# Kernel optimization log

Hardware: AMD Instinct MI355X
Metric: run time of the kernel (lower is better)

The kernel has to match this reference:

```python
import jax, jax.numpy as jnp
import numpy as np

N = 50000
E = 640000
IN_DIM = 23
HID = 128
NUM_CLASS = 12


def setup_inputs() -> dict:
    key = jax.random.key(0)
    ks = jax.random.split(key, 12)
    x = jax.random.normal(ks[0], (N, IN_DIM), dtype=jnp.float32)
    edge_index = jax.random.randint(ks[1], (2, E), 0, N, dtype=jnp.int32)

    def glorot(k, shape):
        fan_in, fan_out = shape
        lim = np.sqrt(6.0 / (fan_in + fan_out)).astype(np.float32)
        return jax.random.uniform(k, shape, jnp.float32, -lim, lim)

    W1 = glorot(ks[2], (IN_DIM, HID)); b1 = jnp.zeros((HID,), jnp.float32)
    W2 = glorot(ks[3], (HID, HID));    b2 = jnp.zeros((HID,), jnp.float32)
    W3 = glorot(ks[4], (HID, HID));    b3 = jnp.zeros((HID,), jnp.float32)
    Wc1 = glorot(ks[5], (HID, 64));    bc1 = jnp.zeros((64,), jnp.float32)
    Wc2 = glorot(ks[6], (64, NUM_CLASS)); bc2 = jnp.zeros((NUM_CLASS,), jnp.float32)
    return {"x": x, "edge_index": edge_index,
            "W1": W1, "b1": b1, "W2": W2, "b2": b2, "W3": W3, "b3": b3,
            "Wc1": Wc1, "bc1": bc1, "Wc2": Wc2, "bc2": bc2}


def _gcn_norm(edge_index, n_nodes):
    # add self loops, compute symmetric normalization D^-1/2 (A+I) D^-1/2
    loop = jnp.arange(n_nodes, dtype=edge_index.dtype)
    src = jnp.concatenate([edge_index[0], loop])
    dst = jnp.concatenate([edge_index[1], loop])
    deg = jax.ops.segment_sum(jnp.ones_like(dst, dtype=jnp.float32), dst,
                              num_segments=n_nodes)
    dinv = jax.lax.rsqrt(deg)  # deg >= 1 due to self loops
    norm = dinv[src] * dinv[dst]  # [E + N]
    return src, dst, norm


def _gcn_layer(h, W, b, src, dst, norm, n_nodes):
    h = h @ W                          # linear (bias applied after aggregation, per PyG)
    msg = h[src] * norm[:, None]       # gather + scale
    out = jax.ops.segment_sum(msg, dst, num_segments=n_nodes)  # scatter-add
    return out + b


def reference(x, edge_index, W1, b1, W2, b2, W3, b3, Wc1, bc1, Wc2, bc2):
    n = x.shape[0]
    src, dst, norm = _gcn_norm(edge_index, n)
    h = jnp.tanh(_gcn_layer(x, W1, b1, src, dst, norm, n))
    h = jnp.tanh(_gcn_layer(h, W2, b2, src, dst, norm, n))
    h = jnp.tanh(_gcn_layer(h, W3, b3, src, dst, norm, n))
    # dropout is identity in eval mode
    out = h @ Wc1 + bc1
    out = out @ Wc2 + bc2
    return out
```

## Files before the change

### kernel.cpp

```cpp
#include <hip/hip_runtime.h>
#include <math.h>

#define NN 50000
#define EE 640000
#define IND 23
#define HID 128
#define MIDD 64
#define NCLS 12
#define NB 49
#define QS 32766.0f
#define INVQS (1.0f / 32766.0f)
#define BSH 7
#define NBK 391
#define CHUNK 4096
#define NPB 157
#define PADB 6250

typedef short short8v __attribute__((ext_vector_type(8)));
typedef float f32x4 __attribute__((ext_vector_type(4)));
typedef unsigned long long u64;

__device__ __forceinline__ short f2bf(float f) {
    unsigned u = __float_as_uint(f);
    unsigned r = (u + 0x7FFFu + ((u >> 16) & 1u)) >> 16;
    return (short)r;
}
__device__ __forceinline__ float bf2f(short s) {
    return __uint_as_float(((unsigned)(unsigned short)s) << 16);
}

__global__ __launch_bounds__(256) void k_pre(const int* __restrict__ dst,
                                             int* __restrict__ cnt,
                                             const float* __restrict__ Wc1,
                                             const float* __restrict__ bc1,
                                             const float* __restrict__ Wc2,
                                             const float* __restrict__ bc2,
                                             float* __restrict__ Wcc,
                                             float* __restrict__ bcc,
                                             const float* __restrict__ W2,
                                             const float* __restrict__ W3,
                                             short* __restrict__ w2hi,
                                             short* __restrict__ w2lo,
                                             short* __restrict__ w3hi,
                                             short* __restrict__ w3lo) {
    const int bid = blockIdx.x;
    const int tid = threadIdx.x;
    if (bid < 2500) {
        int i = bid * 256 + tid;
        if (i < EE) atomicAdd(&cnt[dst[i]], 1);
        return;
    }
    if (bid < 2506) {
        int t = (bid - 2500) * 256 + tid;
        if (t < HID * NCLS) {
            int k = t / NCLS, c = t % NCLS;
            float s = 0.f;
#pragma unroll 8
            for (int j = 0; j < MIDD; ++j) s += Wc1[k * MIDD + j] * Wc2[j * NCLS + c];
            Wcc[t] = s;
        }
        if (t < NCLS) {
            float s = bc2[t];
#pragma unroll 8
            for (int j = 0; j < MIDD; ++j) s += bc1[j] * Wc2[j * NCLS + t];
            bcc[t] = s;
        }
        return;
    }
    int bb = bid - 2506;
    const float* W = (bb < 64) ? W2 : W3;
    short* hi = (bb < 64) ? w2hi : w3hi;
    short* lo = (bb < 64) ? w2lo : w3lo;
    int i = (bb & 63) * 256 + tid;
    int k = i >> 7, c = i & 127;
    float w = W[i];
    short h = f2bf(w);
    short l = f2bf(w - bf2f(h));
    hi[((k >> 3) * 128 + c) * 8 + (k & 7)] = h;
    lo[((k >> 3) * 128 + c) * 8 + (k & 7)] = l;
}

__global__ __launch_bounds__(256) void k_scan_local(const int* __restrict__ cnt,
                                                    int* __restrict__ row_ptr,
                                                    float* __restrict__ dinv,
                                                    int* __restrict__ sums) {
    __shared__ int wtot[4];
    const int tid = threadIdx.x;
    const int wid = tid >> 6, lane = tid & 63;
    const int base = blockIdx.x * 1024 + tid * 4;
    int v[4];
#pragma unroll
    for (int t = 0; t < 4; ++t) {
        int i = base + t;
        v[t] = (i < NN) ? cnt[i] : 0;
        if (i < NN) dinv[i] = rsqrtf((float)v[t] + 1.0f);
    }
    int slocal = v[0] + v[1] + v[2] + v[3];
    int val = slocal;
#pragma unroll
    for (int off = 1; off < 64; off <<= 1) {
        int t = __shfl_up(val, off, 64);
        if (lane >= off) val += t;
    }
    if (lane == 63) wtot[wid] = val;
    __syncthreads();
    int woff = 0;
#pragma unroll
    for (int w = 0; w < 4; ++w) woff += (w < wid) ? wtot[w] : 0;
    int run = woff + val - slocal;
#pragma unroll
    for (int t = 0; t < 4; ++t) {
        int i = base + t;
        if (i < NN) row_ptr[i] = run;
        run += v[t];
    }
    if (tid == 255) sums[blockIdx.x] = woff + val;
}

__global__ __launch_bounds__(256) void k_scan_apply2(int* __restrict__ row_ptr,
                                                     const int* __restrict__ sums,
                                                     int* __restrict__ bcurA) {
    __shared__ int so;
    const int tid = threadIdx.x;
    if (tid < 64) {
        int a = (tid < (int)blockIdx.x) ? sums[tid] : 0;
        int b = (tid < NB) ? sums[tid] : 0;
#pragma unroll
        for (int off = 32; off; off >>= 1) {
            a += __shfl_down(a, off, 64);
            b += __shfl_down(b, off, 64);
        }
        if (tid == 0) {
            so = a;
            if (blockIdx.x == NB - 1) row_ptr[NN] = b;
        }
    }
    __syncthreads();
    const int o = so;
    const int base = blockIdx.x * 1024 + tid * 4;
#pragma unroll
    for (int t = 0; t < 4; ++t) {
        int i = base + t;
        if (i < NN) {
            int rp = row_ptr[i] + o;
            row_ptr[i] = rp;
            if ((i & 127) == 0) bcurA[i >> BSH] = rp;
        }
    }
}

__global__ __launch_bounds__(256) void k_part(const int* __restrict__ src,
                                              const int* __restrict__ dst,
                                              const float* __restrict__ dinv,
                                              int* __restrict__ bcurA,
                                              u64* __restrict__ sw_g,
                                              int* __restrict__ d_g,
                                              const float* __restrict__ x,
                                              float* __restrict__ xp) {
    const int bid = blockIdx.x;
    const int tid = threadIdx.x;
    if (bid >= NPB) {
        int i = (bid - NPB) * 256 + tid;
        int node = i >> 5, f = i & 31;
        xp[i] = (f < IND) ? x[node * IND + f] * dinv[node] : 0.f;
        return;
    }
    __shared__ int hist[NBK], base[NBK], cur[NBK], gb[NBK];
    __shared__ u64 lsw[CHUNK];
    __shared__ int ld[CHUNK];
    const int e0 = bid * CHUNK;
    const int total = min(CHUNK, EE - e0);
    for (int t = tid; t < NBK; t += 256) hist[t] = 0;
    __syncthreads();
    int sv[16], dv[16];
#pragma unroll
    for (int t = 0; t < 16; ++t) {
        int i = e0 + t * 256 + tid;
        if (i < EE) {
            sv[t] = src[i];
            dv[t] = dst[i];
            atomicAdd(&hist[dv[t] >> BSH], 1);
        } else dv[t] = -1;
    }
    __syncthreads();
    if (tid < 64) {
        int carry = 0;
        for (int c = 0; c < NBK; c += 64) {
            int idx = c + tid;
            int v = (idx < NBK) ? hist[idx] : 0;
            int sc = v;
#pragma unroll
            for (int off = 1; off < 64; off <<= 1) {
                int tv = __shfl_up(sc, off, 64);
                if (tid >= off) sc += tv;
            }
            if (idx < NBK) base[idx] = carry + sc - v;
            carry += __shfl(sc, 63, 64);
        }
    }
    __syncthreads();
    for (int t = tid; t < NBK; t += 256) {
        cur[t] = base[t];
        gb[t] = hist[t] ? atomicAdd(&bcurA[t], hist[t]) : 0;
    }
    __syncthreads();
#pragma unroll
    for (int t = 0; t < 16; ++t) {
        if (dv[t] >= 0) {
            int b = dv[t] >> BSH;
            int r = atomicAdd(&cur[b], 1);
            lsw[r] = (unsigned)sv[t] |
                     ((u64)__float_as_uint(dinv[sv[t]]) << 32);
            ld[r] = dv[t];
        }
    }
    __syncthreads();
    for (int j = tid; j < total; j += 256) {
        int d = ld[j];
        int b = d >> BSH;
        int gpos = gb[b] + (j - base[b]);
        sw_g[gpos] = lsw[j];
        d_g[gpos] = d;
    }
}

__global__ __launch_bounds__(256) void k_sort(const int* __restrict__ row_ptr,
                                              const u64* __restrict__ sw_g,
                                              const int* __restrict__ d_g,
                                              u64* __restrict__ e_sn) {
    __shared__ int rloc[129];
    __shared__ int curl[128];
    __shared__ u64 osw[3072];
    const int bid = blockIdx.x, tid = threadIdx.x;
    const int n0 = bid << BSH;
    const int nlast = min(128, NN - n0);
    if (tid <= nlast) rloc[tid] = row_ptr[n0 + tid];
    if (tid < 128) curl[tid] = 0;
    __syncthreads();
    const int rbeg = rloc[0];
    const int cnt = rloc[nlast] - rbeg;
    for (int j = tid; j < cnt; j += 256) {
        int d = d_g[rbeg + j];
        int li = d - n0;
        int r = atomicAdd(&curl[li], 1);
        int pl = (rloc[li] - rbeg) + r;
        u64 v = sw_g[rbeg + j];
        if (pl < 3072) osw[pl] = v;
        else e_sn[rbeg + pl] = v;
    }
    __syncthreads();
    const int lim = min(cnt, 3072);
    for (int j = tid; j < lim; j += 256) e_sn[rbeg + j] = osw[j];
}

__global__ __launch_bounds__(256) void k_l1(const float* __restrict__ xp,
                                            const float* __restrict__ W1,
                                            const float* __restrict__ b1,
                                            const int* __restrict__ row_ptr,
                                            const int2* __restrict__ e_sn,
                                            const float* __restrict__ dinv,
                                            short* __restrict__ outq) {
    const int tid = threadIdx.x;
    const int i = blockIdx.x * 4 + (tid >> 6);
    const int lane = tid & 63;
    const int slot = lane >> 3;
    const int f = lane & 7;
    const float4* xp4 = (const float4*)xp;
    const int beg = row_ptr[i];
    const int deg = row_ptr[i + 1] - beg;
    float4 acc = make_float4(0.f, 0.f, 0.f, 0.f);
    for (int base = 0; base < deg; base += 64) {
        const int cnt = min(64, deg - base);
        int s_l = 0;
        if (lane < cnt) s_l = e_sn[beg + base + lane].x;
        int e = 0;
        for (; e + 8 <= cnt; e += 8) {
            int s = __shfl(s_l, e + slot, 64);
            float4 v = xp4[s * 8 + f];
            acc.x += v.x; acc.y += v.y; acc.z += v.z; acc.w += v.w;
        }
        if (e < cnt) {
            int s = __shfl(s_l, e + slot, 64);
            if (e + slot < cnt) {
                float4 v = xp4[s * 8 + f];
                acc.x += v.x; acc.y += v.y; acc.z += v.z; acc.w += v.w;
            }
        }
    }
#pragma unroll
    for (int off = 32; off >= 8; off >>= 1) {
        acc.x += __shfl_down(acc.x, off, 64);
        acc.y += __shfl_down(acc.y, off, 64);
        acc.z += __shfl_down(acc.z, off, 64);
        acc.w += __shfl_down(acc.w, off, 64);
    }
    const float di = dinv[i];
    if (lane < 8) {
        float4 v = xp4[i * 8 + lane];
        acc.x = (acc.x + v.x) * di; acc.y = (acc.y + v.y) * di;
        acc.z = (acc.z + v.z) * di; acc.w = (acc.w + v.w) * di;
    }
    float a0 = b1[lane], a1 = b1[lane + 64];
#pragma unroll
    for (int k = 0; k < IND; ++k) {
        float comp = ((k & 3) == 0) ? acc.x : ((k & 3) == 1) ? acc.y
                   : ((k & 3) == 2) ? acc.z : acc.w;
        float xk = __shfl(comp, k >> 2, 64);
        a0 += xk * W1[k * HID + lane];
        a1 += xk * W1[k * HID + lane + 64];
    }
    outq[i * HID + lane]      = (short)__float2int_rn(tanhf(a0) * QS);
    outq[i * HID + lane + 64] = (short)__float2int_rn(tanhf(a1) * QS);
}

__global__ __launch_bounds__(256) void k_aggq(const short* __restrict__ hq,
                                              const int* __restrict__ row_ptr,
                                              const int2* __restrict__ e_sn,
                                              const float* __restrict__ dinv,
                                              short8v* __restrict__ ah,
                                              short8v* __restrict__ al) {
    const int tid = threadIdx.x;
    const int i = blockIdx.x * 4 + (tid >> 6);
    const int lane = tid & 63;
    const int slot = lane >> 4;
    const int f = lane & 15;
    const short8v* h8 = (const short8v*)hq;
    const int beg = row_ptr[i];
    const int deg = row_ptr[i + 1] - beg;
    float facc[8];
#pragma unroll
    for (int t = 0; t < 8; ++t) facc[t] = 0.f;
    for (int base = 0; base < deg; base += 64) {
        const int cnt = min(64, deg - base);
        int s_l = 0; float n_l = 0.f;
        if (lane < cnt) {
            int2 sn = e_sn[beg + base + lane];
            s_l = sn.x;
            n_l = __int_as_float(sn.y);
        }
        int e = 0;
#pragma unroll 4
        for (; e + 4 <= cnt; e += 4) {
            int s = __shfl(s_l, e + slot, 64);
            float nr = __shfl(n_l, e + slot, 64);
            short8v v = h8[s * 16 + f];
#pragma unroll
            for (int t = 0; t < 8; ++t) facc[t] += (float)v[t] * nr;
        }
        if (e < cnt) {
            int s = __shfl(s_l, e + slot, 64);
            float nr = __shfl(n_l, e + slot, 64);
            if (e + slot < cnt) {
                short8v v = h8[s * 16 + f];
#pragma unroll
                for (int t = 0; t < 8; ++t) facc[t] += (float)v[t] * nr;
            }
        }
    }
#pragma unroll
    for (int off = 32; off >= 16; off >>= 1)
#pragma unroll
        for (int t = 0; t < 8; ++t) facc[t] += __shfl_down(facc[t], off, 64);
    if (lane < 16) {
        const float di = dinv[i];
        const float sc = di * INVQS;
        short8v v = h8[i * 16 + lane];
        short8v hi8, lo8;
#pragma unroll
        for (int t = 0; t < 8; ++t) {
            float o = (facc[t] + di * (float)v[t]) * sc;
            short h = f2bf(o);
            hi8[t] = h;
            lo8[t] = f2bf(o - bf2f(h));
        }
        const int idx = (i >> 4) * 256 + lane * 16 + (i & 15);
        ah[idx] = hi8;
        al[idx] = lo8;
    }
}

#define GEMM_CORE                                                              \
    const int tid = threadIdx.x;                                               \
    const int lane = tid & 63, wv = tid >> 6;                                  \
    const int g = lane >> 4, c16 = lane & 15;                                  \
    const int rb = blockIdx.x * 16;                                            \
    const int colb = wv * 32;                                                  \
    short8v bh[4][2], bl[4][2];                                                \
    _Pragma("unroll")                                                          \
    for (int t = 0; t < 4; ++t)                                                \
        _Pragma("unroll")                                                      \
        for (int ct = 0; ct < 2; ++ct) {                                       \
            int wi = (t * 4 + g) * 128 + colb + ct * 16 + c16;                 \
            bh[t][ct] = whi8[wi];                                              \
            bl[t][ct] = wlo8[wi];                                              \
        }                                                                      \
    f32x4 acc[2];                                                              \
    acc[0] = f32x4{0.f, 0.f, 0.f, 0.f};                                        \
    acc[1] = f32x4{0.f, 0.f, 0.f, 0.f};                                        \
    const int ab = (rb >> 4) * 256;                                            \
    _Pragma("unroll")                                                          \
    for (int t = 0; t < 4; ++t) {                                              \
        short8v a_h = ah[ab + (t * 4 + g) * 16 + c16];                         \
        short8v a_l = al[ab + (t * 4 + g) * 16 + c16];                         \
        _Pragma("unroll")                                                      \
        for (int ct = 0; ct < 2; ++ct) {                                       \
            acc[ct] = __builtin_amdgcn_mfma_f32_16x16x32_bf16(a_h, bh[t][ct], acc[ct], 0, 0, 0); \
            acc[ct] = __builtin_amdgcn_mfma_f32_16x16x32_bf16(a_h, bl[t][ct], acc[ct], 0, 0, 0); \
            acc[ct] = __builtin_amdgcn_mfma_f32_16x16x32_bf16(a_l, bh[t][ct], acc[ct], 0, 0, 0); \
        }                                                                      \
    }

__global__ __launch_bounds__(256) void k_gemm_q(const short8v* __restrict__ ah,
                                                const short8v* __restrict__ al,
                                                const short8v* __restrict__ whi8,
                                                const short8v* __restrict__ wlo8,
                                                const float* __restrict__ bias,
                                                short* __restrict__ qout) {
    GEMM_CORE
#pragma unroll
    for (int ct = 0; ct < 2; ++ct) {
        const int col = colb + ct * 16 + c16;
        const float bb = bias[col];
#pragma unroll
        for (int r = 0; r < 4; ++r) {
            int nd = rb + 4 * g + r;
            float v = tanhf(acc[ct][r] + bb);
            qout[nd * HID + col] = (short)__float2int_rn(v * QS);
        }
    }
}

__global__ __launch_bounds__(256) void k_gemm_head(const short8v* __restrict__ ah,
                                                   const short8v* __restrict__ al,
                                                   const short8v* __restrict__ whi8,
                                                   const short8v* __restrict__ wlo8,
                                                   const float* __restrict__ bias,
                                                   const float* __restrict__ Wcc,
                                                   const float* __restrict__ bcc,
                                                   float* __restrict__ outp) {
    __shared__ float WccS[HID * NCLS];
    __shared__ float bccS[NCLS];
    __shared__ float psum[4][16][NCLS];
    {
        const int t0 = threadIdx.x;
        for (int t = t0; t < HID * NCLS; t += 256) WccS[t] = Wcc[t];
        if (t0 < NCLS) bccS[t0] = bcc[t0];
    }
    __syncthreads();
    GEMM_CORE
    float part[4][NCLS];
#pragma unroll
    for (int r = 0; r < 4; ++r)
#pragma unroll
        for (int c = 0; c < NCLS; ++c) part[r][c] = 0.f;
#pragma unroll
    for (int ct = 0; ct < 2; ++ct) {
        const int col = colb + ct * 16 + c16;
        const float bb = bias[col];
        const float4* wr = (const float4*)&WccS[col * NCLS];
        float4 wa = wr[0], wb2 = wr[1], wc = wr[2];
#pragma unroll
        for (int r = 0; r < 4; ++r) {
            float v = tanhf(acc[ct][r] + bb);
            part[r][0]  += v * wa.x;  part[r][1]  += v * wa.y;
            part[r][2]  += v * wa.z;  part[r][3]  += v * wa.w;
            part[r][4]  += v * wb2.x; part[r][5]  += v * wb2.y;
            part[r][6]  += v * wb2.z; part[r][7]  += v * wb2.w;
            part[r][8]  += v * wc.x;  part[r][9]  += v * wc.y;
            part[r][10] += v * wc.z;  part[r][11] += v * wc.w;
        }
    }
#pragma unroll
    for (int off = 8; off; off >>= 1)
#pragma unroll
        for (int r = 0; r < 4; ++r)
#pragma unroll
            for (int c = 0; c < NCLS; ++c)
                part[r][c] += __shfl_down(part[r][c], off, 64);
    if (c16 == 0) {
#pragma unroll
        for (int r = 0; r < 4; ++r)
#pragma unroll
            for (int c = 0; c < NCLS; ++c)
                psum[wv][4 * g + r][c] = part[r][c];
    }
    __syncthreads();
    if (tid < 16 * NCLS) {
        int row = tid / NCLS, c = tid % NCLS;
        float s = bccS[c] + psum[0][row][c] + psum[1][row][c]
                + psum[2][row][c] + psum[3][row][c];
        outp[(rb + row) * NCLS + c] = s;
    }
}


extern "C" void kernel_launch(void* const* d_in, const int* in_sizes, int n_in,
                              void* d_out, int out_size, void* d_ws, size_t ws_size,
                              hipStream_t stream) {
    const float* x    = (const float*)d_in[0];
    const int*   edge = (const int*)d_in[1];
    const int*   src  = edge;
    const int*   dst  = edge + EE;
    const float* W1  = (const float*)d_in[2];  const float* b1  = (const float*)d_in[3];
    const float* W2  = (const float*)d_in[4];  const float* b2  = (const float*)d_in[5];
    const float* W3  = (const float*)d_in[6];  const float* b3  = (const float*)d_in[7];
    const float* Wc1 = (const float*)d_in[8];  const float* bc1 = (const float*)d_in[9];
    const float* Wc2 = (const float*)d_in[10]; const float* bc2 = (const float*)d_in[11];
    float* outp = (float*)d_out;

    char* p = (char*)d_ws;
    int*   cnt     = (int*)p;   p += 200064;
    int*   row_ptr = (int*)p;   p += 200064;
    float* dinv    = (float*)p; p += 200064;
    int*   sums    = (int*)p;   p += 256;
    int*   bcurA   = (int*)p;   p += 2048;
    int2*  e_sn    = (int2*)p;  p += (size_t)EE * 8;
    u64*   sw_g    = (u64*)p;   p += (size_t)EE * 8;
    int*   d_g     = (int*)p;   p += (size_t)EE * 4;
    float* xp      = (float*)p; p += (size_t)NN * 32 * 4;
    short* q       = (short*)p; p += (size_t)NN * HID * 2;
    short8v* ah    = (short8v*)p; p += (size_t)3125 * 256 * 16;
    short8v* al    = (short8v*)p; p += (size_t)3125 * 256 * 16;
    float* Wcc     = (float*)p; p += HID * NCLS * 4;
    float* bcc     = (float*)p; p += 256;
    short* w2hi    = (short*)p; p += 32768;
    short* w2lo    = (short*)p; p += 32768;
    short* w3hi    = (short*)p; p += 32768;
    short* w3lo    = (short*)p; p += 32768;

    hipMemsetAsync(cnt, 0, (size_t)NN * 4, stream);
    k_pre        <<<2634, 256, 0, stream>>>(dst, cnt, Wc1, bc1, Wc2, bc2, Wcc, bcc,
                                            W2, W3, w2hi, w2lo, w3hi, w3lo);
    k_scan_local <<<NB, 256, 0, stream>>>(cnt, row_ptr, dinv, sums);
    k_scan_apply2<<<NB, 256, 0, stream>>>(row_ptr, sums, bcurA);
    k_part       <<<NPB + PADB, 256, 0, stream>>>(src, dst, dinv, bcurA,
                                                  sw_g, d_g, x, xp);
    k_sort       <<<NBK, 256, 0, stream>>>(row_ptr, sw_g, d_g, (u64*)e_sn);

    k_l1  <<<NN / 4, 256, 0, stream>>>(xp, W1, b1, row_ptr, e_sn, dinv, q);
    k_aggq     <<<NN / 4, 256, 0, stream>>>(q, row_ptr, e_sn, dinv, ah, al);
    k_gemm_q   <<<NN / 16, 256, 0, stream>>>(ah, al, (const short8v*)w2hi,
                                             (const short8v*)w2lo, b2, q);
    k_aggq     <<<NN / 4, 256, 0, stream>>>(q, row_ptr, e_sn, dinv, ah, al);
    k_gemm_head<<<NN / 16, 256, 0, stream>>>(ah, al, (const short8v*)w3hi,
                                             (const short8v*)w3lo, b3, Wcc, bcc, outp);
}
```

Before: 285.7 us.

## Tile GEMMs over 32 rows, add fast tanh, simplify gather loops, row-major A layout

The GEMM kernels now process 32 rows per block, which reuses the loaded weight fragments across two row tiles and halves the grid, with bounds guards for the tail. The A operands are stored row-major per node instead of the 16-row interleaved layout. The aggregation loops load edge indices directly per slot instead of broadcasting them with shuffles, and tanhf is replaced by an exp-based fast tanh. These cut weight reloads, shuffle overhead and transcendental cost, at the risk of less coalesced A loads and slightly lower tanh accuracy.

```diff
diff --git a/kernel.cpp b/kernel.cpp
--- a/kernel.cpp
+++ b/kernel.cpp
@@ -15,6 +15,7 @@
 #define CHUNK 4096
 #define NPB 157
 #define PADB 6250
+#define GB 1563
 
 typedef short short8v __attribute__((ext_vector_type(8)));
 typedef float f32x4 __attribute__((ext_vector_type(4)));
@@ -27,6 +28,11 @@
 }
 __device__ __forceinline__ float bf2f(short s) {
     return __uint_as_float(((unsigned)(unsigned short)s) << 16);
+}
+__device__ __forceinline__ float fast_tanh(float x) {
+    float t = __expf(-2.f * fabsf(x));
+    float r = (1.f - t) / (1.f + t);
+    return copysignf(r, x);
 }
 
 __global__ __launch_bounds__(256) void k_pre(const int* __restrict__ dst,
@@ -269,22 +275,12 @@
     const int beg = row_ptr[i];
     const int deg = row_ptr[i + 1] - beg;
     float4 acc = make_float4(0.f, 0.f, 0.f, 0.f);
-    for (int base = 0; base < deg; base += 64) {
-        const int cnt = min(64, deg - base);
-        int s_l = 0;
-        if (lane < cnt) s_l = e_sn[beg + base + lane].x;
-        int e = 0;
-        for (; e + 8 <= cnt; e += 8) {
-            int s = __shfl(s_l, e + slot, 64);
+#pragma unroll 4
+    for (int e = 0; e < deg; e += 8) {
+        if (e + slot < deg) {
+            int s = e_sn[beg + e + slot].x;
             float4 v = xp4[s * 8 + f];
             acc.x += v.x; acc.y += v.y; acc.z += v.z; acc.w += v.w;
-        }
-        if (e < cnt) {
-            int s = __shfl(s_l, e + slot, 64);
-            if (e + slot < cnt) {
-                float4 v = xp4[s * 8 + f];
-                acc.x += v.x; acc.y += v.y; acc.z += v.z; acc.w += v.w;
-            }
         }
     }
 #pragma unroll
@@ -309,8 +305,8 @@
         a0 += xk * W1[k * HID + lane];
         a1 += xk * W1[k * HID + lane + 64];
     }
-    outq[i * HID + lane]      = (short)__float2int_rn(tanhf(a0) * QS);
-    outq[i * HID + lane + 64] = (short)__float2int_rn(tanhf(a1) * QS);
+    outq[i * HID + lane]      = (short)__float2int_rn(fast_tanh(a0) * QS);
+    outq[i * HID + lane + 64] = (short)__float2int_rn(fast_tanh(a1) * QS);
 }
 
 __global__ __launch_bounds__(256) void k_aggq(const short* __restrict__ hq,
@@ -330,31 +326,14 @@
     float facc[8];
 #pragma unroll
     for (int t = 0; t < 8; ++t) facc[t] = 0.f;
-    for (int base = 0; base < deg; base += 64) {
-        const int cnt = min(64, deg - base);
-        int s_l = 0; float n_l = 0.f;
-        if (lane < cnt) {
-            int2 sn = e_sn[beg + base + lane];
-            s_l = sn.x;
-            n_l = __int_as_float(sn.y);
-        }
-        int e = 0;
 #pragma unroll 4
-        for (; e + 4 <= cnt; e += 4) {
-            int s = __shfl(s_l, e + slot, 64);
-            float nr = __shfl(n_l, e + slot, 64);
-            short8v v = h8[s * 16 + f];
+    for (int e = 0; e < deg; e += 4) {
+        if (e + slot < deg) {
+            int2 sn = e_sn[beg + e + slot];
+            float nr = __int_as_float(sn.y);
+            short8v v = h8[(size_t)sn.x * 16 + f];
 #pragma unroll
             for (int t = 0; t < 8; ++t) facc[t] += (float)v[t] * nr;
-        }
-        if (e < cnt) {
-            int s = __shfl(s_l, e + slot, 64);
-            float nr = __shfl(n_l, e + slot, 64);
-            if (e + slot < cnt) {
-                short8v v = h8[s * 16 + f];
-#pragma unroll
-                for (int t = 0; t < 8; ++t) facc[t] += (float)v[t] * nr;
-            }
         }
     }
 #pragma unroll
@@ -364,7 +343,7 @@
     if (lane < 16) {
         const float di = dinv[i];
         const float sc = di * INVQS;
-        short8v v = h8[i * 16 + lane];
+        short8v v = h8[(size_t)i * 16 + lane];
         short8v hi8, lo8;
 #pragma unroll
         for (int t = 0; t < 8; ++t) {
@@ -373,42 +352,42 @@
             hi8[t] = h;
             lo8[t] = f2bf(o - bf2f(h));
         }
-        const int idx = (i >> 4) * 256 + lane * 16 + (i & 15);
-        ah[idx] = hi8;
-        al[idx] = lo8;
-    }
-}
-
-#define GEMM_CORE                                                              \
-    const int tid = threadIdx.x;                                               \
-    const int lane = tid & 63, wv = tid >> 6;                                  \
-    const int g = lane >> 4, c16 = lane & 15;                                  \
-    const int rb = blockIdx.x * 16;                                            \
-    const int colb = wv * 32;                                                  \
-    short8v bh[4][2], bl[4][2];                                                \
-    _Pragma("unroll")                                                          \
-    for (int t = 0; t < 4; ++t)                                                \
-        _Pragma("unroll")                                                      \
-        for (int ct = 0; ct < 2; ++ct) {                                       \
-            int wi = (t * 4 + g) * 128 + colb + ct * 16 + c16;                 \
-            bh[t][ct] = whi8[wi];                                              \
-            bl[t][ct] = wlo8[wi];                                              \
-        }                                                                      \
-    f32x4 acc[2];                                                              \
-    acc[0] = f32x4{0.f, 0.f, 0.f, 0.f};                                        \
-    acc[1] = f32x4{0.f, 0.f, 0.f, 0.f};                                        \
-    const int ab = (rb >> 4) * 256;                                            \
-    _Pragma("unroll")                                                          \
-    for (int t = 0; t < 4; ++t) {                                              \
-        short8v a_h = ah[ab + (t * 4 + g) * 16 + c16];                         \
-        short8v a_l = al[ab + (t * 4 + g) * 16 + c16];                         \
-        _Pragma("unroll")                                                      \
-        for (int ct = 0; ct < 2; ++ct) {                                       \
-            acc[ct] = __builtin_amdgcn_mfma_f32_16x16x32_bf16(a_h, bh[t][ct], acc[ct], 0, 0, 0); \
-            acc[ct] = __builtin_amdgcn_mfma_f32_16x16x32_bf16(a_h, bl[t][ct], acc[ct], 0, 0, 0); \
-            acc[ct] = __builtin_amdgcn_mfma_f32_16x16x32_bf16(a_l, bh[t][ct], acc[ct], 0, 0, 0); \
-        }                                                                      \
-    }
+        ah[(size_t)i * 16 + lane] = hi8;
+        al[(size_t)i * 16 + lane] = lo8;
+    }
+}
+
+__device__ __forceinline__ void gemm32(const short8v* __restrict__ ah,
+                                       const short8v* __restrict__ al,
+                                       const short8v* __restrict__ whi8,
+                                       const short8v* __restrict__ wlo8,
+                                       int rb, int colb, int g, int c16,
+                                       f32x4 acc[2][2]) {
+    short8v bh[4][2], bl[4][2];
+#pragma unroll
+    for (int t = 0; t < 4; ++t)
+#pragma unroll
+        for (int ct = 0; ct < 2; ++ct) {
+            int wi = (t * 4 + g) * 128 + colb + ct * 16 + c16;
+            bh[t][ct] = whi8[wi];
+            bl[t][ct] = wlo8[wi];
+        }
+#pragma unroll
+    for (int rt = 0; rt < 2; ++rt) {
+        const size_t arow = (size_t)(rb + rt * 16 + c16) * 16;
+#pragma unroll
+        for (int t = 0; t < 4; ++t) {
+            short8v a_h = ah[arow + t * 4 + g];
+            short8v a_l = al[arow + t * 4 + g];
+#pragma unroll
+            for (int ct = 0; ct < 2; ++ct) {
+                acc[rt][ct] = __builtin_amdgcn_mfma_f32_16x16x32_bf16(a_h, bh[t][ct], acc[rt][ct], 0, 0, 0);
+                acc[rt][ct] = __builtin_amdgcn_mfma_f32_16x16x32_bf16(a_h, bl[t][ct], acc[rt][ct], 0, 0, 0);
+                acc[rt][ct] = __builtin_amdgcn_mfma_f32_16x16x32_bf16(a_l, bh[t][ct], acc[rt][ct], 0, 0, 0);
+            }
+        }
+    }
+}
 
 __global__ __launch_bounds__(256) void k_gemm_q(const short8v* __restrict__ ah,
                                                 const short8v* __restrict__ al,
@@ -416,18 +395,32 @@
                                                 const short8v* __restrict__ wlo8,
                                                 const float* __restrict__ bias,
                                                 short* __restrict__ qout) {
-    GEMM_CORE
-#pragma unroll
-    for (int ct = 0; ct < 2; ++ct) {
-        const int col = colb + ct * 16 + c16;
-        const float bb = bias[col];
-#pragma unroll
-        for (int r = 0; r < 4; ++r) {
-            int nd = rb + 4 * g + r;
-            float v = tanhf(acc[ct][r] + bb);
-            qout[nd * HID + col] = (short)__float2int_rn(v * QS);
-        }
-    }
+    const int tid = threadIdx.x;
+    const int lane = tid & 63, wv = tid >> 6;
+    const int g = lane >> 4, c16 = lane & 15;
+    const int rb = blockIdx.x * 32;
+    const int colb = wv * 32;
+    f32x4 acc[2][2];
+#pragma unroll
+    for (int rt = 0; rt < 2; ++rt)
+#pragma unroll
+        for (int ct = 0; ct < 2; ++ct) acc[rt][ct] = f32x4{0.f, 0.f, 0.f, 0.f};
+    gemm32(ah, al, whi8, wlo8, rb, colb, g, c16, acc);
+#pragma unroll
+    for (int rt = 0; rt < 2; ++rt)
+#pragma unroll
+        for (int ct = 0; ct < 2; ++ct) {
+            const int col = colb + ct * 16 + c16;
+            const float bb = bias[col];
+#pragma unroll
+            for (int r = 0; r < 4; ++r) {
+                int nd = rb + rt * 16 + 4 * g + r;
+                if (nd < NN) {
+                    float v = fast_tanh(acc[rt][ct][r] + bb);
+                    qout[nd * HID + col] = (short)__float2int_rn(v * QS);
+                }
+            }
+        }
 }
 
 __global__ __launch_bounds__(256) void k_gemm_head(const short8v* __restrict__ ah,
@@ -440,56 +433,69 @@
                                                    float* __restrict__ outp) {
     __shared__ float WccS[HID * NCLS];
     __shared__ float bccS[NCLS];
-    __shared__ float psum[4][16][NCLS];
-    {
-        const int t0 = threadIdx.x;
-        for (int t = t0; t < HID * NCLS; t += 256) WccS[t] = Wcc[t];
-        if (t0 < NCLS) bccS[t0] = bcc[t0];
-    }
-    __syncthreads();
-    GEMM_CORE
-    float part[4][NCLS];
-#pragma unroll
-    for (int r = 0; r < 4; ++r)
-#pragma unroll
-        for (int c = 0; c < NCLS; ++c) part[r][c] = 0.f;
-#pragma unroll
-    for (int ct = 0; ct < 2; ++ct) {
-        const int col = colb + ct * 16 + c16;
-        const float bb = bias[col];
-        const float4* wr = (const float4*)&WccS[col * NCLS];
-        float4 wa = wr[0], wb2 = wr[1], wc = wr[2];
-#pragma unroll
-        for (int r = 0; r < 4; ++r) {
-            float v = tanhf(acc[ct][r] + bb);
-            part[r][0]  += v * wa.x;  part[r][1]  += v * wa.y;
-            part[r][2]  += v * wa.z;  part[r][3]  += v * wa.w;
-            part[r][4]  += v * wb2.x; part[r][5]  += v * wb2.y;
-            part[r][6]  += v * wb2.z; part[r][7]  += v * wb2.w;
-            part[r][8]  += v * wc.x;  part[r][9]  += v * wc.y;
-            part[r][10] += v * wc.z;  part[r][11] += v * wc.w;
-        }
-    }
-#pragma unroll
-    for (int off = 8; off; off >>= 1)
+    __shared__ float psum[4][32][NCLS];
+    const int tid = threadIdx.x;
+    for (int t = tid; t < HID * NCLS; t += 256) WccS[t] = Wcc[t];
+    if (tid < NCLS) bccS[tid] = bcc[tid];
+    __syncthreads();
+    const int lane = tid & 63, wv = tid >> 6;
+    const int g = lane >> 4, c16 = lane & 15;
+    const int rb = blockIdx.x * 32;
+    const int colb = wv * 32;
+    f32x4 acc[2][2];
+#pragma unroll
+    for (int rt = 0; rt < 2; ++rt)
+#pragma unroll
+        for (int ct = 0; ct < 2; ++ct) acc[rt][ct] = f32x4{0.f, 0.f, 0.f, 0.f};
+    gemm32(ah, al, whi8, wlo8, rb, colb, g, c16, acc);
+#pragma unroll
+    for (int rt = 0; rt < 2; ++rt) {
+        float part[4][NCLS];
 #pragma unroll
         for (int r = 0; r < 4; ++r)
 #pragma unroll
-            for (int c = 0; c < NCLS; ++c)
-                part[r][c] += __shfl_down(part[r][c], off, 64);
-    if (c16 == 0) {
-#pragma unroll
-        for (int r = 0; r < 4; ++r)
-#pragma unroll
-            for (int c = 0; c < NCLS; ++c)
-                psum[wv][4 * g + r][c] = part[r][c];
-    }
-    __syncthreads();
-    if (tid < 16 * NCLS) {
-        int row = tid / NCLS, c = tid % NCLS;
-        float s = bccS[c] + psum[0][row][c] + psum[1][row][c]
-                + psum[2][row][c] + psum[3][row][c];
-        outp[(rb + row) * NCLS + c] = s;
+            for (int c = 0; c < NCLS; ++c) part[r][c] = 0.f;
+#pragma unroll
+        for (int ct = 0; ct < 2; ++ct) {
+            const int col = colb + ct * 16 + c16;
+            const float bb = bias[col];
+            const float4* wr = (const float4*)&WccS[col * NCLS];
+            float4 wa = wr[0], wb2 = wr[1], wc = wr[2];
+#pragma unroll
+            for (int r = 0; r < 4; ++r) {
+                float v = fast_tanh(acc[rt][ct][r] + bb);
+                part[r][0]  += v * wa.x;  part[r][1]  += v * wa.y;
+                part[r][2]  += v * wa.z;  part[r][3]  += v * wa.w;
+                part[r][4]  += v * wb2.x; part[r][5]  += v * wb2.y;
+                part[r][6]  += v * wb2.z; part[r][7]  += v * wb2.w;
+                part[r][8]  += v * wc.x;  part[r][9]  += v * wc.y;
+                part[r][10] += v * wc.z;  part[r][11] += v * wc.w;
+            }
+        }
+#pragma unroll
+        for (int off = 8; off; off >>= 1)
+#pragma unroll
+            for (int r = 0; r < 4; ++r)
+#pragma unroll
+                for (int c = 0; c < NCLS; ++c)
+                    part[r][c] += __shfl_down(part[r][c], off, 64);
+        if (c16 == 0) {
+#pragma unroll
+            for (int r = 0; r < 4; ++r)
+#pragma unroll
+                for (int c = 0; c < NCLS; ++c)
+                    psum[wv][rt * 16 + 4 * g + r][c] = part[r][c];
+        }
+    }
+    __syncthreads();
+    for (int t2 = tid; t2 < 32 * NCLS; t2 += 256) {
+        int row = t2 / NCLS, c = t2 % NCLS;
+        int nd = rb + row;
+        if (nd < NN) {
+            float s = bccS[c] + psum[0][row][c] + psum[1][row][c]
+                    + psum[2][row][c] + psum[3][row][c];
+            outp[nd * NCLS + c] = s;
+        }
     }
 }
 
@@ -519,8 +525,8 @@
     int*   d_g     = (int*)p;   p += (size_t)EE * 4;
     float* xp      = (float*)p; p += (size_t)NN * 32 * 4;
     short* q       = (short*)p; p += (size_t)NN * HID * 2;
-    short8v* ah    = (short8v*)p; p += (size_t)3125 * 256 * 16;
-    short8v* al    = (short8v*)p; p += (size_t)3125 * 256 * 16;
+    short8v* ah    = (short8v*)p; p += (size_t)(NN + 16) * 256;
+    short8v* al    = (short8v*)p; p += (size_t)(NN + 16) * 256;
     float* Wcc     = (float*)p; p += HID * NCLS * 4;
     float* bcc     = (float*)p; p += 256;
     short* w2hi    = (short*)p; p += 32768;
@@ -539,9 +545,9 @@
 
     k_l1  <<<NN / 4, 256, 0, stream>>>(xp, W1, b1, row_ptr, e_sn, dinv, q);
     k_aggq     <<<NN / 4, 256, 0, stream>>>(q, row_ptr, e_sn, dinv, ah, al);
-    k_gemm_q   <<<NN / 16, 256, 0, stream>>>(ah, al, (const short8v*)w2hi,
-                                             (const short8v*)w2lo, b2, q);
+    k_gemm_q   <<<GB, 256, 0, stream>>>(ah, al, (const short8v*)w2hi,
+                                        (const short8v*)w2lo, b2, q);
     k_aggq     <<<NN / 4, 256, 0, stream>>>(q, row_ptr, e_sn, dinv, ah, al);
-    k_gemm_head<<<NN / 16, 256, 0, stream>>>(ah, al, (const short8v*)w3hi,
-                                             (const short8v*)w3lo, b3, Wcc, bcc, outp);
-}
+    k_gemm_head<<<GB, 256, 0, stream>>>(ah, al, (const short8v*)w3hi,
+                                        (const short8v*)w3lo, b3, Wcc, bcc, outp);
+}
```

Measured after the change: 307.3 us. 1.08x slower.

## Use row-major A layout for MFMA GEMM, fast exp-based tanh, stream weight loads

Applied to the files above, without the earlier changes.

Swaps tanhf for an __expf-based tanh in the layer-1, GEMM and head epilogues to cut transcendental cost. k_aggq now writes the bf16 hi/lo split activations row-major, and the GEMM core reads A fragments strided by row instead of the earlier 16-row tiled layout. B fragments are now loaded inside the MFMA loop rather than preloaded into registers. The A reads in the GEMM may be less coalesced, and fast_tanh adds a little rounding error that could slightly change the quantized output.

```diff
diff --git a/kernel.cpp b/kernel.cpp
--- a/kernel.cpp
+++ b/kernel.cpp
@@ -15,6 +15,7 @@
 #define CHUNK 4096
 #define NPB 157
 #define PADB 6250
+#define GB16 3125
 
 typedef short short8v __attribute__((ext_vector_type(8)));
 typedef float f32x4 __attribute__((ext_vector_type(4)));
@@ -27,6 +28,11 @@
 }
 __device__ __forceinline__ float bf2f(short s) {
     return __uint_as_float(((unsigned)(unsigned short)s) << 16);
+}
+__device__ __forceinline__ float fast_tanh(float x) {
+    float t = __expf(-2.f * fabsf(x));
+    float r = (1.f - t) / (1.f + t);
+    return copysignf(r, x);
 }
 
 __global__ __launch_bounds__(256) void k_pre(const int* __restrict__ dst,
@@ -309,8 +315,8 @@
         a0 += xk * W1[k * HID + lane];
         a1 += xk * W1[k * HID + lane + 64];
     }
-    outq[i * HID + lane]      = (short)__float2int_rn(tanhf(a0) * QS);
-    outq[i * HID + lane + 64] = (short)__float2int_rn(tanhf(a1) * QS);
+    outq[i * HID + lane]      = (short)__float2int_rn(fast_tanh(a0) * QS);
+    outq[i * HID + lane + 64] = (short)__float2int_rn(fast_tanh(a1) * QS);
 }
 
 __global__ __launch_bounds__(256) void k_aggq(const short* __restrict__ hq,
@@ -343,7 +349,7 @@
         for (; e + 4 <= cnt; e += 4) {
             int s = __shfl(s_l, e + slot, 64);
             float nr = __shfl(n_l, e + slot, 64);
-            short8v v = h8[s * 16 + f];
+            short8v v = h8[(size_t)s * 16 + f];
 #pragma unroll
             for (int t = 0; t < 8; ++t) facc[t] += (float)v[t] * nr;
         }
@@ -351,7 +357,7 @@
             int s = __shfl(s_l, e + slot, 64);
             float nr = __shfl(n_l, e + slot, 64);
             if (e + slot < cnt) {
-                short8v v = h8[s * 16 + f];
+                short8v v = h8[(size_t)s * 16 + f];
 #pragma unroll
                 for (int t = 0; t < 8; ++t) facc[t] += (float)v[t] * nr;
             }
@@ -364,7 +370,7 @@
     if (lane < 16) {
         const float di = dinv[i];
         const float sc = di * INVQS;
-        short8v v = h8[i * 16 + lane];
+        short8v v = h8[(size_t)i * 16 + lane];
         short8v hi8, lo8;
 #pragma unroll
         for (int t = 0; t < 8; ++t) {
@@ -373,40 +379,33 @@
             hi8[t] = h;
             lo8[t] = f2bf(o - bf2f(h));
         }
-        const int idx = (i >> 4) * 256 + lane * 16 + (i & 15);
-        ah[idx] = hi8;
-        al[idx] = lo8;
-    }
-}
-
-#define GEMM_CORE                                                              \
+        ah[(size_t)i * 16 + lane] = hi8;
+        al[(size_t)i * 16 + lane] = lo8;
+    }
+}
+
+#define GEMM_CORE16                                                            \
     const int tid = threadIdx.x;                                               \
     const int lane = tid & 63, wv = tid >> 6;                                  \
     const int g = lane >> 4, c16 = lane & 15;                                  \
     const int rb = blockIdx.x * 16;                                            \
     const int colb = wv * 32;                                                  \
-    short8v bh[4][2], bl[4][2];                                                \
+    f32x4 acc[2];                                                              \
+    acc[0] = f32x4{0.f, 0.f, 0.f, 0.f};                                        \
+    acc[1] = f32x4{0.f, 0.f, 0.f, 0.f};                                        \
+    const size_t arow = (size_t)(rb + c16) * 16;                               \
     _Pragma("unroll")                                                          \
-    for (int t = 0; t < 4; ++t)                                                \
+    for (int t = 0; t < 4; ++t) {                                              \
+        short8v a_h = ah[arow + t * 4 + g];                                    \
+        short8v a_l = al[arow + t * 4 + g];                                    \
         _Pragma("unroll")                                                      \
         for (int ct = 0; ct < 2; ++ct) {                                       \
             int wi = (t * 4 + g) * 128 + colb + ct * 16 + c16;                 \
-            bh[t][ct] = whi8[wi];                                              \
-            bl[t][ct] = wlo8[wi];                                              \
-        }                                                                      \
-    f32x4 acc[2];                                                              \
-    acc[0] = f32x4{0.f, 0.f, 0.f, 0.f};                                        \
-    acc[1] = f32x4{0.f, 0.f, 0.f, 0.f};                                        \
-    const int ab = (rb >> 4) * 256;                                            \
-    _Pragma("unroll")                                                          \
-    for (int t = 0; t < 4; ++t) {                                              \
-        short8v a_h = ah[ab + (t * 4 + g) * 16 + c16];                         \
-        short8v a_l = al[ab + (t * 4 + g) * 16 + c16];                         \
-        _Pragma("unroll")                                                      \
-        for (int ct = 0; ct < 2; ++ct) {                                       \
-            acc[ct] = __builtin_amdgcn_mfma_f32_16x16x32_bf16(a_h, bh[t][ct], acc[ct], 0, 0, 0); \
-            acc[ct] = __builtin_amdgcn_mfma_f32_16x16x32_bf16(a_h, bl[t][ct], acc[ct], 0, 0, 0); \
-            acc[ct] = __builtin_amdgcn_mfma_f32_16x16x32_bf16(a_l, bh[t][ct], acc[ct], 0, 0, 0); \
+            short8v bh = whi8[wi];                                             \
+            short8v bl = wlo8[wi];                                             \
+            acc[ct] = __builtin_amdgcn_mfma_f32_16x16x32_bf16(a_h, bh, acc[ct], 0, 0, 0); \
+            acc[ct] = __builtin_amdgcn_mfma_f32_16x16x32_bf16(a_h, bl, acc[ct], 0, 0, 0); \
+            acc[ct] = __builtin_amdgcn_mfma_f32_16x16x32_bf16(a_l, bh, acc[ct], 0, 0, 0); \
         }                                                                      \
     }
 
@@ -416,7 +415,7 @@
                                                 const short8v* __restrict__ wlo8,
                                                 const float* __restrict__ bias,
                                                 short* __restrict__ qout) {
-    GEMM_CORE
+    GEMM_CORE16
 #pragma unroll
     for (int ct = 0; ct < 2; ++ct) {
         const int col = colb + ct * 16 + c16;
@@ -424,7 +423,7 @@
 #pragma unroll
         for (int r = 0; r < 4; ++r) {
             int nd = rb + 4 * g + r;
-            float v = tanhf(acc[ct][r] + bb);
+            float v = fast_tanh(acc[ct][r] + bb);
             qout[nd * HID + col] = (short)__float2int_rn(v * QS);
         }
     }
@@ -447,7 +446,7 @@
         if (t0 < NCLS) bccS[t0] = bcc[t0];
     }
     __syncthreads();
-    GEMM_CORE
+    GEMM_CORE16
     float part[4][NCLS];
 #pragma unroll
     for (int r = 0; r < 4; ++r)
@@ -461,7 +460,7 @@
         float4 wa = wr[0], wb2 = wr[1], wc = wr[2];
 #pragma unroll
         for (int r = 0; r < 4; ++r) {
-            float v = tanhf(acc[ct][r] + bb);
+            float v = fast_tanh(acc[ct][r] + bb);
             part[r][0]  += v * wa.x;  part[r][1]  += v * wa.y;
             part[r][2]  += v * wa.z;  part[r][3]  += v * wa.w;
             part[r][4]  += v * wb2.x; part[r][5]  += v * wb2.y;
@@ -519,8 +518,8 @@
     int*   d_g     = (int*)p;   p += (size_t)EE * 4;
     float* xp      = (float*)p; p += (size_t)NN * 32 * 4;
     short* q       = (short*)p; p += (size_t)NN * HID * 2;
-    short8v* ah    = (short8v*)p; p += (size_t)3125 * 256 * 16;
-    short8v* al    = (short8v*)p; p += (size_t)3125 * 256 * 16;
+    short8v* ah    = (short8v*)p; p += (size_t)(NN + 16) * 256;
+    short8v* al    = (short8v*)p; p += (size_t)(NN + 16) * 256;
     float* Wcc     = (float*)p; p += HID * NCLS * 4;
     float* bcc     = (float*)p; p += 256;
     short* w2hi    = (short*)p; p += 32768;
@@ -539,9 +538,9 @@
 
     k_l1  <<<NN / 4, 256, 0, stream>>>(xp, W1, b1, row_ptr, e_sn, dinv, q);
     k_aggq     <<<NN / 4, 256, 0, stream>>>(q, row_ptr, e_sn, dinv, ah, al);
-    k_gemm_q   <<<NN / 16, 256, 0, stream>>>(ah, al, (const short8v*)w2hi,
-                                             (const short8v*)w2lo, b2, q);
+    k_gemm_q   <<<GB16, 256, 0, stream>>>(ah, al, (const short8v*)w2hi,
+                                          (const short8v*)w2lo, b2, q);
     k_aggq     <<<NN / 4, 256, 0, stream>>>(q, row_ptr, e_sn, dinv, ah, al);
-    k_gemm_head<<<NN / 16, 256, 0, stream>>>(ah, al, (const short8v*)w3hi,
-                                             (const short8v*)w3lo, b3, Wcc, bcc, outp);
-}
+    k_gemm_head<<<GB16, 256, 0, stream>>>(ah, al, (const short8v*)w3hi,
+                                          (const short8v*)w3lo, b3, Wcc, bcc, outp);
+}
```

Result: slower. 297.3 us (+4.1%).
